# Kernel tuning notes

Hardware: AMD Instinct MI355X
Metric: run time of the kernel (lower is better)

Reference implementation:

```python
import jax, jax.numpy as jnp
import numpy as np

EPS = 1e-05
K = 32


def _knn_idx(xyz_B3N, k):
    # negative squared pairwise distance: -||xi||^2 + 2 xi.xj - ||xj||^2
    inner = 2.0 * jnp.einsum('bdn,bdm->bnm', xyz_B3N, xyz_B3N)  # [B,N,N]
    xx = jnp.sum(xyz_B3N ** 2, axis=1)  # [B,N]
    pd = inner - xx[:, :, None] - xx[:, None, :]
    _, idx = jax.lax.top_k(pd, k)  # [B,N,k] nearest (largest negative dist)
    return idx


def setup_inputs() -> dict:
    key = jax.random.key(0)
    k1, k2 = jax.random.split(key)
    B, N, C = 16, 4096, 64
    xyz_B3N = jax.random.normal(k1, (B, 3, N), dtype=jnp.float32)
    feats_BNC = jax.random.normal(k2, (B, N, C), dtype=jnp.float32)
    alpha = jnp.ones((C,), dtype=jnp.float32)
    beta = jnp.zeros((C,), dtype=jnp.float32)
    return {"xyz_B3N": xyz_B3N, "feats_BNC": feats_BNC, "alpha": alpha, "beta": beta}


def reference(xyz_B3N, feats_BNC, alpha, beta):
    idx = _knn_idx(xyz_B3N, K)  # [B,N,k]
    # gather neighbor features directly: [B,N,k,C]
    neigh = jax.vmap(lambda f, i: f[i])(feats_BNC, idx)
    offset = neigh - feats_BNC[:, :, None, :]  # [B,N,k,C]
    sigma = jnp.mean(offset ** 2)  # global scalar
    gaed = (offset / (sigma + EPS)) * alpha + beta
    pooled = jnp.max(gaed, axis=2)  # [B,N,C]
    return pooled
```

## Files before the change

kernel.cpp:

```cpp
#include <hip/hip_runtime.h>
#include <float.h>

#define BB 16
#define NN 4096
#define CC 64
#define KNN 32
#define NSLICE 16
#define SSZ 256
#define CKEEP 8
#define NQ 65536


__device__ __forceinline__ int lane_rank(unsigned long long m) {
    return __builtin_amdgcn_mbcnt_hi((unsigned)(m >> 32),
           __builtin_amdgcn_mbcnt_lo((unsigned)m, 0u));
}

__device__ __forceinline__ unsigned med3u(unsigned a, unsigned b, unsigned c) {
    unsigned d;
    asm("v_med3_u32 %0, %1, %2, %3" : "=v"(d) : "v"(a), "v"(b), "v"(c));
    return d;
}

#define UCHAIN8 \
  h07=med3u(ky,h07,h06); h06=med3u(ky,h06,h05); h05=med3u(ky,h05,h04); \
  h04=med3u(ky,h04,h03); h03=med3u(ky,h03,h02); h02=med3u(ky,h02,h01); \
  h01=med3u(ky,h01,h00); h00=(h00>ky)?h00:ky;

__global__ __launch_bounds__(256) void prep_kernel(
        const float* __restrict__ xyz, float4* __restrict__ pts4,
        int* __restrict__ flag_cnt) {
#pragma clang fp contract(off)
    const int p = blockIdx.x * 256 + threadIdx.x;
    if (p == 0) flag_cnt[0] = 0;
    const int b = p >> 12;
    const int i = p & (NN - 1);
    const float* xb = xyz + (size_t)b * (3 * NN);
    float x = xb[i], y = xb[NN + i], z = xb[2 * NN + i];
    float xx = ((x * x) + (y * y)) + (z * z);
    pts4[p] = make_float4(x, y, z, xx);
}

__global__ __launch_bounds__(256) void knn_select_kernel(
        const float4* __restrict__ pts4, unsigned* __restrict__ val_buf) {
#pragma clang fp contract(off)
    __shared__ float4 pts[SSZ];
    const int tid = threadIdx.x;
    const int blk = blockIdx.x;
    const int s = blk & 15;
    const int g = (blk >> 4) & 15;
    const int b = blk >> 8;
    const float4* pb = pts4 + (b << 12);

    pts[tid] = pb[(s << 8) | tid];
    const int q = (g << 8) | tid;
    const float4 qp = pb[q];
    const float qx = qp.x, qy = qp.y, qz = qp.z;
    const float nqxx = -qp.w;
    __syncthreads();

    unsigned h00=0,h01=0,h02=0,h03=0,h04=0,h05=0,h06=0,h07=0;
    const unsigned ibase = 4095u - (unsigned)(s << 8);
#pragma unroll 4
    for (int j = 0; j < SSZ; ++j) {
        float4 cp = pts[j];
        float dot = __builtin_fmaf(qz, cp.z, __builtin_fmaf(qy, cp.y, qx * cp.x));
        float pd = __builtin_fmaf(2.0f, dot, nqxx) - cp.w;
        unsigned u = __float_as_uint(pd);
        unsigned mono = u ^ (unsigned)(((int)u >> 31) | 0x80000000);
        unsigned ky = (mono & 0xFFFFF000u) | (ibase - (unsigned)j);
        UCHAIN8
    }

    const int qg = (b << 12) | q;
    unsigned* vp = val_buf + (size_t)(s * CKEEP) * NQ + qg;
#define ST(t, ht) vp[(size_t)(t) * NQ] = ht;
    ST(0,h00) ST(1,h01) ST(2,h02) ST(3,h03)
    ST(4,h04) ST(5,h05) ST(6,h06) ST(7,h07)
#undef ST
}

__global__ __launch_bounds__(64) void knn_merge_kernel(
        const unsigned* __restrict__ val_buf, int* __restrict__ idx_out,
        int* __restrict__ flag_list, int* __restrict__ flag_cnt) {
    __shared__ unsigned lv[64 * 129];
    const int tid = threadIdx.x;
    const int qg = blockIdx.x * 64 + tid;
    unsigned* my = lv + tid * 129;
    for (int t = 0; t < 128; ++t) my[t] = val_buf[(size_t)t * NQ + qg];

    int p0=0,p1=0,p2=0,p3=0,p4=0,p5=0,p6=0,p7=0,
        p8=0,p9=0,p10=0,p11=0,p12=0,p13=0,p14=0,p15=0;
    unsigned v0 =my[0],  v1 =my[8],  v2 =my[16],  v3 =my[24];
    unsigned v4 =my[32], v5 =my[40], v6 =my[48],  v7 =my[56];
    unsigned v8 =my[64], v9 =my[72], v10=my[80],  v11=my[88];
    unsigned v12=my[96], v13=my[104],v14=my[112], v15=my[120];
    int* outp = idx_out + (size_t)qg * KNN;
    unsigned key32 = 0u, key33 = 0u;
    for (int step = 0; step < 33; ++step) {
        unsigned best = v0; int bp = 0;
        if (v1  > best) { best = v1;  bp = 1; }
        if (v2  > best) { best = v2;  bp = 2; }
        if (v3  > best) { best = v3;  bp = 3; }
        if (v4  > best) { best = v4;  bp = 4; }
        if (v5  > best) { best = v5;  bp = 5; }
        if (v6  > best) { best = v6;  bp = 6; }
        if (v7  > best) { best = v7;  bp = 7; }
        if (v8  > best) { best = v8;  bp = 8; }
        if (v9  > best) { best = v9;  bp = 9; }
        if (v10 > best) { best = v10; bp = 10; }
        if (v11 > best) { best = v11; bp = 11; }
        if (v12 > best) { best = v12; bp = 12; }
        if (v13 > best) { best = v13; bp = 13; }
        if (v14 > best) { best = v14; bp = 14; }
        if (v15 > best) { best = v15; bp = 15; }
        if (step == 32) { key33 = best; break; }
        outp[step] = 4095 - (int)(best & 4095u);
        if (step == 31) key32 = best;
        if      (bp==0)  { ++p0;  v0  = (p0 <8)?my[p0]      :0u; }
        else if (bp==1)  { ++p1;  v1  = (p1 <8)?my[8+p1]    :0u; }
        else if (bp==2)  { ++p2;  v2  = (p2 <8)?my[16+p2]   :0u; }
        else if (bp==3)  { ++p3;  v3  = (p3 <8)?my[24+p3]   :0u; }
        else if (bp==4)  { ++p4;  v4  = (p4 <8)?my[32+p4]   :0u; }
        else if (bp==5)  { ++p5;  v5  = (p5 <8)?my[40+p5]   :0u; }
        else if (bp==6)  { ++p6;  v6  = (p6 <8)?my[48+p6]   :0u; }
        else if (bp==7)  { ++p7;  v7  = (p7 <8)?my[56+p7]   :0u; }
        else if (bp==8)  { ++p8;  v8  = (p8 <8)?my[64+p8]   :0u; }
        else if (bp==9)  { ++p9;  v9  = (p9 <8)?my[72+p9]   :0u; }
        else if (bp==10) { ++p10; v10 = (p10<8)?my[80+p10]  :0u; }
        else if (bp==11) { ++p11; v11 = (p11<8)?my[88+p11]  :0u; }
        else if (bp==12) { ++p12; v12 = (p12<8)?my[96+p12]  :0u; }
        else if (bp==13) { ++p13; v13 = (p13<8)?my[104+p13] :0u; }
        else if (bp==14) { ++p14; v14 = (p14<8)?my[112+p14] :0u; }
        else             { ++p15; v15 = (p15<8)?my[120+p15] :0u; }
    }

    bool flag = ((key32 >> 12) == (key33 >> 12));
    for (int sl = 0; sl < 16; ++sl)
        flag = flag || (my[sl * 8 + 7] >= key33);
    if (flag) {
        int pos = atomicAdd(flag_cnt, 1);
        flag_list[pos] = qg;
    }
}

__global__ __launch_bounds__(256) void knn_fallback_kernel(
        const float* __restrict__ xyz, const int* __restrict__ flag_list,
        const int* __restrict__ flag_cnt, int* __restrict__ idx_out) {
#pragma clang fp contract(off)
    const int nflag = flag_cnt[0];
    const int lane = threadIdx.x & 63;
    const int wid = (blockIdx.x * 256 + threadIdx.x) >> 6;
    const int nw = (gridDim.x * 256) >> 6;
    for (int w = wid; w < nflag; w += nw) {
        const int qg = flag_list[w];
        const int b = qg >> 12;
        const int q = qg & (NN - 1);
        const float* xb = xyz + (size_t)b * (3 * NN);
        const float qx = xb[q], qy = xb[NN + q], qz = xb[2 * NN + q];
        const float qxx = ((qx * qx) + (qy * qy)) + (qz * qz);
        const float nqxx = -qxx;

        unsigned key[64];
#pragma unroll
        for (int i = 0; i < 64; ++i) {
            const int j = (i << 6) | lane;
            float x = xb[j], y = xb[NN + j], z = xb[2 * NN + j];
            float xxc = ((x * x) + (y * y)) + (z * z);
            float dot = __builtin_fmaf(qz, z, __builtin_fmaf(qy, y, qx * x));
            float pd = __builtin_fmaf(2.0f, dot, nqxx) - xxc;
            unsigned u = __float_as_uint(pd);
            key[i] = u ^ (unsigned)(((int)u >> 31) | 0x80000000);
        }

        unsigned cur = 0u;
        for (int bit = 31; bit >= 0; --bit) {
            const unsigned cand = cur | (1u << bit);
            int c = 0;
#pragma unroll
            for (int i = 0; i < 64; ++i) c += (key[i] >= cand) ? 1 : 0;
#pragma unroll
            for (int o = 32; o >= 1; o >>= 1) c += __shfl_xor(c, o, 64);
            if (c >= 32) cur = cand;
        }

        int ge = 0;
#pragma unroll
        for (int i = 0; i < 64; ++i) {
            ge += (key[i] > cur) ? 1 : 0;
            ge += (key[i] == cur) ? 0x10000 : 0;
        }
#pragma unroll
        for (int o = 32; o >= 1; o >>= 1) ge += __shfl_xor(ge, o, 64);
        const int gt_total = ge & 0xFFFF;
        const int budget = min(ge >> 16, 32 - gt_total);

        int* outp = idx_out + (size_t)qg * KNN;
        int slot = 0, neq = 0;
#pragma unroll
        for (int i = 0; i < 64; ++i) {
            const bool isgt = key[i] > cur;
            const bool iseq = key[i] == cur;
            const unsigned long long mgt = __ballot(isgt);
            const unsigned long long meq = __ballot(iseq);
            if (isgt) outp[slot + lane_rank(mgt)] = (i << 6) | lane;
            if (iseq) {
                const int r = neq + lane_rank(meq);
                if (r < budget) outp[gt_total + r] = (i << 6) | lane;
            }
            slot += __builtin_popcountll(mgt);
            neq += __builtin_popcountll(meq);
        }
    }
}

__global__ __launch_bounds__(256) void gather_minmax_kernel(
        const float* __restrict__ feats, const int* __restrict__ idx_in,
        float* __restrict__ mx_buf, float* __restrict__ mn_buf,
        double* __restrict__ partials) {
    const int tid = threadIdx.x;
    const int w = tid >> 6;
    const int lane = tid & 63;
    const int q = blockIdx.x * 4 + w;
    const int b = q >> 12;
    const float* fb = feats + (size_t)b * (NN * CC);
    const float center = feats[(size_t)q * CC + lane];
    const int* ip = idx_in + (size_t)q * KNN;

    float mx = -FLT_MAX, mn = FLT_MAX;
    double ss = 0.0;
#pragma unroll 4
    for (int k = 0; k < KNN; ++k) {
        int nb = ip[k];
        float v = fb[(size_t)nb * CC + lane];
        float off = v - center;
        mx = fmaxf(mx, off);
        mn = fminf(mn, off);
        double od = (double)off;
        ss = fma(od, od, ss);
    }
    mx_buf[(size_t)q * CC + lane] = mx;
    mn_buf[(size_t)q * CC + lane] = mn;

#pragma unroll
    for (int o = 32; o >= 1; o >>= 1) ss += __shfl_down(ss, o, 64);
    __shared__ double wsum[4];
    if (lane == 0) wsum[w] = ss;
    __syncthreads();
    if (tid == 0) partials[blockIdx.x] = (wsum[0] + wsum[1]) + (wsum[2] + wsum[3]);
}

__global__ __launch_bounds__(256) void sigma_kernel(const double* __restrict__ partials,
                                                    float* __restrict__ sigma) {
    __shared__ double red[256];
    double s = 0.0;
    for (int i = threadIdx.x; i < 16384; i += 256) s += partials[i];
    red[threadIdx.x] = s;
    __syncthreads();
    for (int o = 128; o >= 1; o >>= 1) {
        if (threadIdx.x < o) red[threadIdx.x] += red[threadIdx.x + o];
        __syncthreads();
    }
    if (threadIdx.x == 0) sigma[0] = (float)(red[0] * (1.0 / 134217728.0));
}

__global__ __launch_bounds__(256) void finalize_kernel(
        const float* __restrict__ mx_buf, const float* __restrict__ mn_buf,
        const float* __restrict__ alpha, const float* __restrict__ beta,
        const float* __restrict__ sigma, float* __restrict__ out) {
#pragma clang fp contract(off)
    const int e = blockIdx.x * 256 + threadIdx.x;
    const int c = e & (CC - 1);
    const float s = sigma[0] + 1e-5f;
    const float a = alpha[c];
    const float bt = beta[c];
    const float off = (a >= 0.f) ? mx_buf[e] : mn_buf[e];
    const float t = off / s;
    out[e] = (t * a) + bt;
}

extern "C" void kernel_launch(void* const* d_in, const int* in_sizes, int n_in,
                              void* d_out, int out_size, void* d_ws, size_t ws_size,
                              hipStream_t stream) {
    (void)in_sizes; (void)n_in; (void)out_size; (void)ws_size;
    const float* xyz   = (const float*)d_in[0];
    const float* feats = (const float*)d_in[1];
    const float* alpha = (const float*)d_in[2];
    const float* beta  = (const float*)d_in[3];
    float* out = (float*)d_out;

    char* ws = (char*)d_ws;
    unsigned* val_buf  = (unsigned*)ws;
    float*    mx_buf   = (float*)ws;
    float*    mn_buf   = (float*)(ws + 16777216);
    int*      idx_buf  = (int*)(ws + 33554432);
    int*      flag_list= (int*)(ws + 41943040);
    int*      flag_cnt = (int*)(ws + 42205184);
    float4*   pts4     = (float4*)(ws + 42205200);
    double*   partials = (double*)(ws + 42205200);
    float*    sigma    = (float*)(ws + 42336272);

    prep_kernel<<<NQ / 256, 256, 0, stream>>>(xyz, pts4, flag_cnt);
    knn_select_kernel<<<BB * 16 * NSLICE, 256, 0, stream>>>(pts4, val_buf);
    knn_merge_kernel<<<NQ / 64, 64, 0, stream>>>(val_buf, idx_buf,
                                                 flag_list, flag_cnt);
    knn_fallback_kernel<<<256, 256, 0, stream>>>(xyz, flag_list, flag_cnt,
                                                 idx_buf);
    gather_minmax_kernel<<<NQ / 4, 256, 0, stream>>>(feats, idx_buf, mx_buf,
                                                     mn_buf, partials);
    sigma_kernel<<<1, 256, 0, stream>>>(partials, sigma);
    finalize_kernel<<<(NQ * CC) / 256, 256, 0, stream>>>(mx_buf, mn_buf, alpha,
                                                         beta, sigma, out);
}
```

Measured before the change: 348.9 us.

## Replace per-element med3 insertion chain with batched sorting-network top-8 merge

The KNN select loop now processes candidates in batches of 8. Each batch is sorted with a 19-comparator network, combined with the running top-8 through a bitonic max step, and the result is re-sorted with a bitonic merge. This replaces the per-candidate 8-op med3 insertion chain. The key encoding also changes: distances are clamped to at most zero and bit-inverted instead of using the sign-flip transform. Workspace offsets are realigned so pts4 sits on a 64-byte boundary and sigma gets more room. The min/max work per candidate is roughly similar, so any benefit relies on more instruction-level parallelism from independent comparators.

```diff
diff --git a/kernel.cpp b/kernel.cpp
--- a/kernel.cpp
+++ b/kernel.cpp
@@ -16,16 +16,13 @@
            __builtin_amdgcn_mbcnt_lo((unsigned)m, 0u));
 }
 
-__device__ __forceinline__ unsigned med3u(unsigned a, unsigned b, unsigned c) {
-    unsigned d;
-    asm("v_med3_u32 %0, %1, %2, %3" : "=v"(d) : "v"(a), "v"(b), "v"(c));
-    return d;
-}
-
-#define UCHAIN8 \
-  h07=med3u(ky,h07,h06); h06=med3u(ky,h06,h05); h05=med3u(ky,h05,h04); \
-  h04=med3u(ky,h04,h03); h03=med3u(ky,h03,h02); h02=med3u(ky,h02,h01); \
-  h01=med3u(ky,h01,h00); h00=(h00>ky)?h00:ky;
+__device__ __forceinline__ unsigned umaxu(unsigned a, unsigned b) {
+    return a > b ? a : b;
+}
+__device__ __forceinline__ unsigned uminu(unsigned a, unsigned b) {
+    return a < b ? a : b;
+}
+#define CE(a, b) { unsigned _mx = umaxu(a, b); b = uminu(a, b); a = _mx; }
 
 __global__ __launch_bounds__(256) void prep_kernel(
         const float* __restrict__ xyz, float4* __restrict__ pts4,
@@ -59,24 +56,40 @@
     const float nqxx = -qp.w;
     __syncthreads();
 
-    unsigned h00=0,h01=0,h02=0,h03=0,h04=0,h05=0,h06=0,h07=0;
+    unsigned h0=0,h1=0,h2=0,h3=0,h4=0,h5=0,h6=0,h7=0;
     const unsigned ibase = 4095u - (unsigned)(s << 8);
-#pragma unroll 4
-    for (int j = 0; j < SSZ; ++j) {
-        float4 cp = pts[j];
-        float dot = __builtin_fmaf(qz, cp.z, __builtin_fmaf(qy, cp.y, qx * cp.x));
-        float pd = __builtin_fmaf(2.0f, dot, nqxx) - cp.w;
-        unsigned u = __float_as_uint(pd);
-        unsigned mono = u ^ (unsigned)(((int)u >> 31) | 0x80000000);
-        unsigned ky = (mono & 0xFFFFF000u) | (ibase - (unsigned)j);
-        UCHAIN8
+    for (int j0 = 0; j0 < SSZ; j0 += 8) {
+        unsigned k0,k1,k2,k3,k4,k5,k6,k7;
+#define KY(ji, dst) { \
+        float4 cp = pts[j0 + ji]; \
+        float dot = __builtin_fmaf(qz, cp.z, \
+                    __builtin_fmaf(qy, cp.y, qx * cp.x)); \
+        float pd = __builtin_fmaf(2.0f, dot, nqxx) - cp.w; \
+        pd = fminf(pd, 0.0f); \
+        dst = (~__float_as_uint(pd) & 0xFFFFF000u) \
+              | (ibase - (unsigned)(j0 + ji)); }
+        KY(0,k0) KY(1,k1) KY(2,k2) KY(3,k3)
+        KY(4,k4) KY(5,k5) KY(6,k6) KY(7,k7)
+#undef KY
+        CE(k0,k1) CE(k2,k3) CE(k0,k2) CE(k1,k3) CE(k1,k2)
+        CE(k4,k5) CE(k6,k7) CE(k4,k6) CE(k5,k7) CE(k5,k6)
+        CE(k0,k4) CE(k1,k5) CE(k2,k6) CE(k3,k7)
+        CE(k2,k4) CE(k3,k5)
+        CE(k1,k2) CE(k3,k4) CE(k5,k6)
+        h0 = umaxu(h0, k7); h1 = umaxu(h1, k6);
+        h2 = umaxu(h2, k5); h3 = umaxu(h3, k4);
+        h4 = umaxu(h4, k3); h5 = umaxu(h5, k2);
+        h6 = umaxu(h6, k1); h7 = umaxu(h7, k0);
+        CE(h0,h4) CE(h1,h5) CE(h2,h6) CE(h3,h7)
+        CE(h0,h2) CE(h1,h3) CE(h4,h6) CE(h5,h7)
+        CE(h0,h1) CE(h2,h3) CE(h4,h5) CE(h6,h7)
     }
 
     const int qg = (b << 12) | q;
     unsigned* vp = val_buf + (size_t)(s * CKEEP) * NQ + qg;
 #define ST(t, ht) vp[(size_t)(t) * NQ] = ht;
-    ST(0,h00) ST(1,h01) ST(2,h02) ST(3,h03)
-    ST(4,h04) ST(5,h05) ST(6,h06) ST(7,h07)
+    ST(0,h0) ST(1,h1) ST(2,h2) ST(3,h3)
+    ST(4,h4) ST(5,h5) ST(6,h6) ST(7,h7)
 #undef ST
 }
 
@@ -296,9 +309,9 @@
     int*      idx_buf  = (int*)(ws + 33554432);
     int*      flag_list= (int*)(ws + 41943040);
     int*      flag_cnt = (int*)(ws + 42205184);
-    float4*   pts4     = (float4*)(ws + 42205200);
-    double*   partials = (double*)(ws + 42205200);
-    float*    sigma    = (float*)(ws + 42336272);
+    float4*   pts4     = (float4*)(ws + 42205248);
+    double*   partials = (double*)(ws + 42205248);
+    float*    sigma    = (float*)(ws + 43254784);
 
     prep_kernel<<<NQ / 256, 256, 0, stream>>>(xyz, pts4, flag_cnt);
     knn_select_kernel<<<BB * 16 * NSLICE, 256, 0, stream>>>(pts4, val_buf);
```

Measured after the change: 353.1 us. No clear change (+1.2%).
